# Kernel optimization log

Hardware: AMD Instinct MI355X
Metric: run time of the kernel (lower is better)

## Reference

```python
import jax, jax.numpy as jnp
from jax import lax
import numpy as np

B, N, DIM = 2, 2048, 1024
HEADS, DIM_HEAD = 16, 64
KERNELS = (0, 3, 5, 7)
GROUPS = len(KERNELS)
HPG = HEADS // GROUPS          # heads per group = 4
CG = HPG * DIM_HEAD            # channels per group for depthwise conv = 256
INNER = HEADS * DIM_HEAD       # 1024


def _alibi_slopes(n):
    # power-of-2 branch of LearnedAlibiPosBias._get_slopes (n=4 here)
    start = 2.0 ** (-(2.0 ** -(np.log2(n) - 3)))
    return np.array([start * start ** i for i in range(n)], dtype=np.float32)


def setup_inputs() -> dict:
    key = jax.random.key(0)
    ks = jax.random.split(key, 24)
    d = {}
    d['x'] = jax.random.normal(ks[0], (B, N, DIM), jnp.float32)
    d['ln_gamma'] = jnp.ones((DIM,), jnp.float32)
    d['ln_beta'] = jnp.zeros((DIM,), jnp.float32)
    d['w_qkv'] = jax.random.normal(ks[1], (3 * INNER, DIM), jnp.float32) * 0.02
    i = 2
    for p in ('q', 'k', 'v'):
        for ksz in (3, 5, 7):
            d[f'dw{p}_w{ksz}'] = jax.random.normal(ks[i], (CG, 1, ksz), jnp.float32) * 0.1; i += 1
            d[f'dw{p}_b{ksz}'] = jax.random.normal(ks[i], (CG,), jnp.float32) * 0.02; i += 1
    # learned alibi slopes, initialized to the standard ALiBi values per group
    sl = _alibi_slopes(HPG).reshape(1, HPG, 1, 1)
    d['slopes'] = jnp.asarray(np.tile(sl, (GROUPS, 1, 1, 1)))
    d['w_out'] = jax.random.normal(ks[20], (DIM, INNER), jnp.float32) * 0.02
    return d


def _dw_causal_conv(xg, w, b, ksz):
    # xg: (B, CG, N); depthwise causal conv, left pad ksz-1
    xg = jnp.pad(xg, ((0, 0), (0, 0), (ksz - 1, 0)))
    out = lax.conv_general_dilated(xg, w, (1,), 'VALID',
                                   feature_group_count=CG,
                                   dimension_numbers=('NCH', 'OIH', 'NCH'))
    return out + b[None, :, None]


def _grouped_conv(t, w3, b3, w5, b5, w7, b7):
    # t: (B, INNER, N) channels laid out head-major; group g = channels [g*CG,(g+1)*CG)
    parts = [t[:, :CG]]  # group 0: kernel_size 0 -> Identity
    for i, (w, b, ksz) in enumerate(((w3, b3, 3), (w5, b5, 5), (w7, b7, 7))):
        parts.append(_dw_causal_conv(t[:, (i + 1) * CG:(i + 2) * CG], w, b, ksz))
    out = jnp.concatenate(parts, axis=1)                      # (B, INNER, N)
    out = out.reshape(B, HEADS, DIM_HEAD, N)
    return jnp.transpose(out, (0, 1, 3, 2))                   # (B, H, N, Dh)


def _forward(x, ln_gamma, ln_beta, w_qkv,
             dwq_w3, dwq_b3, dwq_w5, dwq_b5, dwq_w7, dwq_b7,
             dwk_w3, dwk_b3, dwk_w5, dwk_b5, dwk_w7, dwk_b7,
             dwv_w3, dwv_b3, dwv_w5, dwv_b5, dwv_w7, dwv_b7,
             slopes, w_out):
    scale = DIM_HEAD ** -0.5
    mu = jnp.mean(x, axis=-1, keepdims=True)
    var = jnp.var(x, axis=-1, keepdims=True)
    h = (x - mu) * lax.rsqrt(var + 1e-5) * ln_gamma + ln_beta   # (B, N, DIM)
    qkv = jnp.einsum('bnd,ed->ben', h, w_qkv)                   # (B, 3*INNER, N)
    q, k, v = jnp.split(qkv, 3, axis=1)
    q = _grouped_conv(q, dwq_w3, dwq_b3, dwq_w5, dwq_b5, dwq_w7, dwq_b7)
    k = _grouped_conv(k, dwk_w3, dwk_b3, dwk_w5, dwk_b5, dwk_w7, dwk_b7)
    v = _grouped_conv(v, dwv_w3, dwv_b3, dwv_w5, dwv_b5, dwv_w7, dwv_b7)
    sim = jnp.einsum('bhid,bhjd->bhij', q * scale, k)           # (B, H, N, N)
    idx = jnp.arange(N)
    dist = -jnp.abs(idx[None, :] - idx[:, None]).astype(sim.dtype)  # (N, N)
    bias = slopes.reshape(HEADS, 1, 1) * dist[None]             # (H, N, N)
    sim = sim + bias[None]
    causal = idx[None, :] > idx[:, None]                        # strictly future
    sim = jnp.where(causal[None, None], -jnp.finfo(sim.dtype).max, sim)
    attn = jax.nn.softmax(sim, axis=-1)
    out = jnp.einsum('bhij,bhjd->bhid', attn, v)                # (B, H, N, Dh)
    out = jnp.transpose(out, (0, 2, 1, 3)).reshape(B, N, INNER)
    return jnp.einsum('bne,de->bnd', out, w_out)


def reference(x, ln_gamma, ln_beta, w_qkv,
              dwq_w3, dwq_b3, dwq_w5, dwq_b5, dwq_w7, dwq_b7,
              dwk_w3, dwk_b3, dwk_w5, dwk_b5, dwk_w7, dwk_b7,
              dwv_w3, dwv_b3, dwv_w5, dwv_b5, dwv_w7, dwv_b7,
              slopes, w_out):
    return _forward(x, ln_gamma, ln_beta, w_qkv,
                    dwq_w3, dwq_b3, dwq_w5, dwq_b5, dwq_w7, dwq_b7,
                    dwk_w3, dwk_b3, dwk_w5, dwk_b5, dwk_w7, dwk_b7,
                    dwv_w3, dwv_b3, dwv_w5, dwv_b5, dwv_w7, dwv_b7,
                    slopes, w_out)
```

## Files before the change

kernel.cpp:

```cpp
#include <hip/hip_runtime.h>
#include <hip/hip_bf16.h>
#include <stdint.h>

typedef __bf16 bf8 __attribute__((ext_vector_type(8)));
typedef float  f4  __attribute__((ext_vector_type(4)));

constexpr int BATCH  = 2;
constexpr int SEQ    = 2048;
constexpr int DMODEL = 1024;
constexpr int NH     = 16;
constexpr int DHEAD  = 64;
constexpr int E3     = 3072;

static __device__ __forceinline__ f4 mfma16(bf8 a, bf8 b, f4 c){
  return __builtin_amdgcn_mfma_f32_16x16x32_bf16(a, b, c, 0, 0, 0);
}
static __device__ __forceinline__ uint32_t pack2(float a, float b){
  union { __bf16 h[2]; uint32_t u; } p;
  p.h[0] = (__bf16)a; p.h[1] = (__bf16)b;
  return p.u;
}
typedef const __attribute__((address_space(1))) uint32_t g_u32;
typedef __attribute__((address_space(3))) uint32_t l_u32;
static __device__ __forceinline__ void glds16(const __bf16* g, __bf16* l){
  __builtin_amdgcn_global_load_lds((g_u32*)g, (l_u32*)l, 16, 0, 0);
}

__global__ __launch_bounds__(256) void prep_kernel(const float* __restrict__ x,
                                                   const float* __restrict__ gam,
                                                   const float* __restrict__ bet,
                                                   __bf16* __restrict__ h,
                                                   const float* __restrict__ wq,
                                                   __bf16* __restrict__ wqb){
  int bid = blockIdx.x;
  int tid = threadIdx.x;
  if(bid >= BATCH*SEQ){
    int i = ((bid - BATCH*SEQ) * 256 + tid) * 4;
    float4 v = *(const float4*)(wq + i);
    __bf16 o[4] = {(__bf16)v.x, (__bf16)v.y, (__bf16)v.z, (__bf16)v.w};
    *(uint2*)(wqb + i) = *(const uint2*)o;
    return;
  }
  int row = bid;
  const float* xr = x + (size_t)row * DMODEL;
  float4 v = *(const float4*)(xr + tid*4);
  float s = v.x + v.y + v.z + v.w;
  float ss = v.x*v.x + v.y*v.y + v.z*v.z + v.w*v.w;
#pragma unroll
  for(int m=1;m<64;m<<=1){ s += __shfl_xor(s, m); ss += __shfl_xor(ss, m); }
  __shared__ float sm[8];
  int wid = tid >> 6;
  if((tid & 63) == 0){ sm[wid] = s; sm[4+wid] = ss; }
  __syncthreads();
  s  = sm[0]+sm[1]+sm[2]+sm[3];
  ss = sm[4]+sm[5]+sm[6]+sm[7];
  float mu  = s * (1.f/DMODEL);
  float var = ss * (1.f/DMODEL) - mu*mu;
  float r = rsqrtf(var + 1e-5f);
  float4 g = *(const float4*)(gam + tid*4);
  float4 bb = *(const float4*)(bet + tid*4);
  __bf16 o[4] = { (__bf16)((v.x-mu)*r*g.x + bb.x), (__bf16)((v.y-mu)*r*g.y + bb.y),
                  (__bf16)((v.z-mu)*r*g.z + bb.z), (__bf16)((v.w-mu)*r*g.w + bb.w) };
  *(uint2*)(h + (size_t)row*DMODEL + tid*4) = *(uint2*)o;
}

template<typename CT>
__global__ __launch_bounds__(256) void gemm_nt(const __bf16* __restrict__ A,
                                               const __bf16* __restrict__ Bm,
                                               CT* __restrict__ C,
                                               int M, int Ncols, int K){
  __shared__ __align__(16) __bf16 smem[4*128*32];
  __bf16* As0 = smem;
  __bf16* Bs0 = smem + 2*128*32;
  int m0 = blockIdx.y * 128, n0 = blockIdx.x * 128;
  int tid = threadIdx.x;
  int lane = tid & 63, wid = tid >> 6;
  int quad = lane >> 4, l15 = lane & 15;
  int wm = (wid >> 1) * 64, wn = (wid & 1) * 64;
  f4 acc[4][4] = {};
  int r0 = wid*32 + (lane >> 2);
  int cofs = (lane & 3) * 8;
  const __bf16* ag = A  + (size_t)(m0 + r0) * K + cofs;
  const __bf16* bg = Bm + (size_t)(n0 + r0) * K + cofs;
  const int d0 = (wid*32)*32, d1 = (wid*32+16)*32;
  const size_t rowskip = (size_t)16 * K;
  glds16(ag,           As0 + d0);
  glds16(ag + rowskip, As0 + d1);
  glds16(bg,           Bs0 + d0);
  glds16(bg + rowskip, Bs0 + d1);
  __syncthreads();
  int cur = 0;
  for(int k0 = 0; k0 < K; k0 += 32){
    int k1 = k0 + 32;
    if(k1 < K){
      int nb = cur ^ 1;
      glds16(ag + k1,           As0 + nb*128*32 + d0);
      glds16(ag + rowskip + k1, As0 + nb*128*32 + d1);
      glds16(bg + k1,           Bs0 + nb*128*32 + d0);
      glds16(bg + rowskip + k1, Bs0 + nb*128*32 + d1);
    }
    const __bf16* AsC = As0 + cur*128*32;
    const __bf16* BsC = Bs0 + cur*128*32;
    bf8 af[4], bfr[4];
#pragma unroll
    for(int i=0;i<4;i++){
      af[i]  = *(const bf8*)&AsC[(wm + i*16 + l15)*32 + quad*8];
      bfr[i] = *(const bf8*)&BsC[(wn + i*16 + l15)*32 + quad*8];
    }
#pragma unroll
    for(int mi=0;mi<4;mi++)
#pragma unroll
      for(int ni=0;ni<4;ni++)
        acc[mi][ni] = mfma16(af[mi], bfr[ni], acc[mi][ni]);
    __syncthreads();
    cur ^= 1;
  }
  if constexpr (sizeof(CT) == 2){
    __bf16* scr = smem;
    uint32_t* sp = (uint32_t*)smem;
#pragma unroll
    for(int qq=0; qq<4; qq++){
      __syncthreads();
      if((wid>>1) == (qq>>1)){
        int mi0 = (qq & 1) * 2;
#pragma unroll
        for(int mm=0; mm<2; mm++){
          int mi = mi0 + mm;
#pragma unroll
          for(int ni=0; ni<4; ni++)
#pragma unroll
            for(int r=0; r<4; r++){
              int lr = (mi - mi0)*16 + quad*4 + r;
              scr[lr*136 + wn + ni*16 + l15] = (__bf16)acc[mi][ni][r];
            }
        }
      }
      __syncthreads();
#pragma unroll
      for(int it=0; it<2; it++){
        int idx = it*256 + tid;
        int row = idx >> 4;
        int ck  = idx & 15;
        uint4 v = { sp[row*68 + ck*4 + 0], sp[row*68 + ck*4 + 1],
                    sp[row*68 + ck*4 + 2], sp[row*68 + ck*4 + 3] };
        *(uint4*)(C + (size_t)(m0 + qq*32 + row)*Ncols + n0 + ck*8) = v;
      }
    }
  } else {
    float* scr = (float*)smem;
#pragma unroll
    for(int qq=0; qq<4; qq++){
      __syncthreads();
      if((wid>>1) == (qq>>1)){
        int mi0 = (qq & 1) * 2;
#pragma unroll
        for(int mm=0; mm<2; mm++){
          int mi = mi0 + mm;
#pragma unroll
          for(int ni=0; ni<4; ni++)
#pragma unroll
            for(int r=0; r<4; r++){
              int lr = (mi - mi0)*16 + quad*4 + r;
              scr[lr*136 + wn + ni*16 + l15] = acc[mi][ni][r];
            }
        }
      }
      __syncthreads();
#pragma unroll
      for(int it=0; it<4; it++){
        int idx = it*256 + tid;
        int row = idx >> 5;
        int ck  = idx & 31;
        float4 v = { scr[row*136 + ck*4 + 0], scr[row*136 + ck*4 + 1],
                     scr[row*136 + ck*4 + 2], scr[row*136 + ck*4 + 3] };
        *(float4*)(C + (size_t)(m0 + qq*32 + row)*Ncols + n0 + ck*4) = v;
      }
    }
  }
}

__global__ __launch_bounds__(256) void conv_kernel(const __bf16* __restrict__ qkv,
    __bf16* __restrict__ qo, __bf16* __restrict__ ko, __bf16* __restrict__ vt,
    const float* qw3,const float* qb3,const float* qw5,const float* qb5,const float* qw7,const float* qb7,
    const float* kw3,const float* kb3,const float* kw5,const float* kb5,const float* kw7,const float* kb7,
    const float* vw3,const float* vb3,const float* vw5,const float* vb5,const float* vw7,const float* vb7){
  __shared__ __align__(16) __bf16 tile[72*256];
  int nc = blockIdx.x;
  int ec = blockIdx.y;
  int b  = blockIdx.z;
  int tid = threadIdx.x;
  int n0 = nc * 64;
  {
    int rrow = tid >> 5;
    int ccol = (tid & 31) * 8;
    const __bf16* src = qkv + (size_t)b*SEQ*E3 + ec*256 + ccol;
#pragma unroll
    for(int p=0;p<9;p++){
      int row = p*8 + rrow;
      int n = n0 - 8 + row;
      uint4 v = {0u,0u,0u,0u};
      if(n >= 0) v = *(const uint4*)(src + (size_t)n*E3);
      *(uint4*)&tile[row*256 + ccol] = v;
    }
  }
  __syncthreads();
  int p = ec >> 2;
  int g = ec & 3;
  float w0=0.f,w1=0.f,w2=0.f,w3=0.f,w4=0.f,w5=0.f,w6=0.f,bias=0.f;
  if(g == 1){
    const float* wp = (p==0)? qw3 : (p==1)? kw3 : vw3;
    const float* bp = (p==0)? qb3 : (p==1)? kb3 : vb3;
    w0 = wp[tid*3+0]; w1 = wp[tid*3+1]; w2 = wp[tid*3+2]; bias = bp[tid];
  } else if(g == 2){
    const float* wp = (p==0)? qw5 : (p==1)? kw5 : vw5;
    const float* bp = (p==0)? qb5 : (p==1)? kb5 : vb5;
    w0 = wp[tid*5+0]; w1 = wp[tid*5+1]; w2 = wp[tid*5+2];
    w3 = wp[tid*5+3]; w4 = wp[tid*5+4]; bias = bp[tid];
  } else if(g == 3){
    const float* wp = (p==0)? qw7 : (p==1)? kw7 : vw7;
    const float* bp = (p==0)? qb7 : (p==1)? kb7 : vb7;
    w0 = wp[tid*7+0]; w1 = wp[tid*7+1]; w2 = wp[tid*7+2]; w3 = wp[tid*7+3];
    w4 = wp[tid*7+4]; w5 = wp[tid*7+5]; w6 = wp[tid*7+6]; bias = bp[tid];
  }
  float x0 = (float)tile[2*256 + tid];
  float x1 = (float)tile[3*256 + tid];
  float x2 = (float)tile[4*256 + tid];
  float x3 = (float)tile[5*256 + tid];
  float x4 = (float)tile[6*256 + tid];
  float x5 = (float)tile[7*256 + tid];
#define CONV_STEP(cur, o)                                                      \
  { if(g == 0)      o = (cur);                                                 \
    else if(g == 1) o = w0*x4 + w1*x5 + w2*(cur) + bias;                       \
    else if(g == 2) o = w0*x2 + w1*x3 + w2*x4 + w3*x5 + w4*(cur) + bias;       \
    else            o = w0*x0 + w1*x1 + w2*x2 + w3*x3 + w4*x4 + w5*x5          \
                        + w6*(cur) + bias;                                     \
    x0=x1; x1=x2; x2=x3; x3=x4; x4=x5; x5=(cur); }
  if(p == 2){
    uint32_t vout[32];
#pragma unroll
    for(int blk=0; blk<8; blk++){
#pragma unroll
      for(int up=0; up<4; up++){
        float ca = (float)tile[(8 + blk*8 + up*2    )*256 + tid];
        float oa; CONV_STEP(ca, oa);
        float cb = (float)tile[(8 + blk*8 + up*2 + 1)*256 + tid];
        float ob; CONV_STEP(cb, ob);
        vout[blk*4 + up] = pack2(oa, ob);
      }
    }
    __syncthreads();
    uint32_t* ot = (uint32_t*)tile;
#pragma unroll
    for(int j=0;j<32;j++) ot[tid*33 + j] = vout[j];
    __syncthreads();
#pragma unroll
    for(int it=0; it<8; it++){
      int idx = it*256 + tid;
      int ch  = idx >> 3;
      int ncq = idx & 7;
      uint4 val = { ot[ch*33 + ncq*4 + 0], ot[ch*33 + ncq*4 + 1],
                    ot[ch*33 + ncq*4 + 2], ot[ch*33 + ncq*4 + 3] };
      int hh2 = g*4 + (ch >> 6);
      int dh2 = ch & 63;
      *(uint4*)(vt + ((size_t)((b*NH + hh2)*DHEAD + dh2))*SEQ + n0 + ncq*8) = val;
    }
  } else {
    int hh = g*4 + (tid >> 6);
    int dh = tid & 63;
    __bf16* outp = (p==0) ? qo : ko;
    __bf16* op = outp + ((size_t)(b*NH + hh)*SEQ)*DHEAD + dh;
#pragma unroll 8
    for(int dn=0; dn<64; dn++){
      float cur = (float)tile[(8+dn)*256 + tid];
      float o; CONV_STEP(cur, o);
      op[(size_t)(n0+dn)*DHEAD] = (__bf16)o;
    }
  }
#undef CONV_STEP
}

__global__ __launch_bounds__(256, 3) void attn_kernel(const __bf16* __restrict__ Qin,
                                                      const __bf16* __restrict__ Kin,
                                                      const __bf16* __restrict__ Vtin,
                                                      const float* __restrict__ slopes,
                                                      __bf16* __restrict__ Oout,
                                                      const float* __restrict__ wsrc,
                                                      __bf16* __restrict__ wdst){
  __shared__ __align__(16) __bf16 Ks[2][64*64];
  __shared__ __align__(16) __bf16 Vts[2][64*64];
  __shared__ __align__(16) __bf16 Ps[4][16*72];
  __shared__ float Al[4][16];
  int bid = blockIdx.x;
  int tid = threadIdx.x;
  if(bid >= 1024){
    int i = ((bid - 1024) * 256 + tid) * 4;
    float4 v = *(const float4*)(wsrc + i);
    __bf16 o[4] = {(__bf16)v.x, (__bf16)v.y, (__bf16)v.z, (__bf16)v.w};
    *(uint2*)(wdst + i) = *(const uint2*)o;
    return;
  }
  int qi = 31 - (bid >> 5);
  int by = (bid & 7) + ((bid >> 3) & 3) * 8;
  int b  = by >> 4, hh = by & 15;
  int lane = tid & 63, w = tid >> 6;
  int quad = lane >> 4, l15 = lane & 15;
  const __bf16* qb  = Qin  + (size_t)by * SEQ * DHEAD;
  const __bf16* kb  = Kin  + (size_t)by * SEQ * DHEAD;
  const __bf16* vtb = Vtin + (size_t)by * DHEAD * SEQ;
  const float L2E = 1.4426950408889634f;
  float slope = slopes[hh];
  const float c1 = 0.125f * L2E;
  float c2 = slope * L2E;
  float cjb[16];
#pragma unroll
  for(int jt=0;jt<4;jt++)
#pragma unroll
    for(int r=0;r<4;r++)
      cjb[jt*4+r] = c2 * (float)(jt*16 + quad*4 + r);

  int sxq0 = ((quad     ^ (l15 & 7)) << 3);
  int sxq1 = (((quad+4) ^ (l15 & 7)) << 3);

  int r8 = lane >> 3;
  int c8 = lane & 7;
  int sw = (c8 ^ r8) * 8;
  const __bf16* ksrc = kb  + (size_t)r8*DHEAD + sw;
  const __bf16* vsrc = vtb + (size_t)r8*SEQ  + sw;
  int g0 = w*2, g1 = w*2 + 1;
  const size_t kg0o = (size_t)g0*8*DHEAD, kg1o = (size_t)g1*8*DHEAD;
  const size_t vg0o = (size_t)g0*8*SEQ,   vg1o = (size_t)g1*8*SEQ;

  int q0 = qi * 64;
  int nst = qi + 1;
  int i0 = q0 + w*16;
  int i  = i0 + l15;
  bf8 aq0 = *(const bf8*)(qb + (size_t)i*DHEAD + quad*8);
  bf8 aq1 = *(const bf8*)(qb + (size_t)i*DHEAD + 32 + quad*8);
  f4 oacc[4] = {};
  float l_ = 0.f;
  glds16(ksrc + kg0o, &Ks[0][g0*512]);
  glds16(ksrc + kg1o, &Ks[0][g1*512]);
  glds16(vsrc + vg0o, &Vts[0][g0*512]);
  glds16(vsrc + vg1o, &Vts[0][g1*512]);
  __syncthreads();
  int cur = 0;
  for(int t=0; t<nst; t++){
    int j0 = t*64;
    bool pf = (t+1) < nst;
    if(pf){
      int nb = cur ^ 1;
      size_t off = (size_t)(t+1)*64;
      glds16(ksrc + off*DHEAD + kg0o, &Ks[nb][g0*512]);
      glds16(ksrc + off*DHEAD + kg1o, &Ks[nb][g1*512]);
      glds16(vsrc + vg0o + off,       &Vts[nb][g0*512]);
      glds16(vsrc + vg1o + off,       &Vts[nb][g1*512]);
    }
    const __bf16* KsC  = Ks[cur];
    const __bf16* VtsC = Vts[cur];
    f4 s[4] = {};
    __builtin_amdgcn_s_setprio(1);
#pragma unroll
    for(int jt=0;jt<4;jt++){
      bf8 ak0 = *(const bf8*)&KsC[(jt*16+l15)*64 + sxq0];
      bf8 ak1 = *(const bf8*)&KsC[(jt*16+l15)*64 + sxq1];
      s[jt] = mfma16(ak0, aq0, s[jt]);
      s[jt] = mfma16(ak1, aq1, s[jt]);
    }
    __builtin_amdgcn_s_setprio(0);
    bf8 bv[2][4];
#pragma unroll
    for(int jk=0;jk<2;jk++)
#pragma unroll
      for(int nd=0;nd<4;nd++)
        bv[jk][nd] = *(const bf8*)&VtsC[(nd*16+l15)*64 + (((jk*4+quad) ^ (l15&7)) << 3)];
    float sv[4][4];
    if(t < nst-1){
      float cdi = c2 * (float)(i - j0) + 8.0f;
#pragma unroll
      for(int jt=0;jt<4;jt++)
#pragma unroll
        for(int r=0;r<4;r++)
          sv[jt][r] = fmaf(s[jt][r], c1, cjb[jt*4+r] - cdi);
    } else {
#pragma unroll
      for(int jt=0;jt<4;jt++)
#pragma unroll
        for(int r=0;r<4;r++){
          int j = j0 + jt*16 + quad*4 + r;
          int d = i - j;
          float val = fmaf(s[jt][r], c1, -fmaf(c2, (float)d, 8.0f));
          sv[jt][r] = (d < 0) ? -1e30f : val;
        }
    }
    float lsum = 0.f;
#pragma unroll
    for(int jt=0;jt<4;jt++){
      float p0 = __builtin_amdgcn_exp2f(sv[jt][0]);
      float p1 = __builtin_amdgcn_exp2f(sv[jt][1]);
      float p2 = __builtin_amdgcn_exp2f(sv[jt][2]);
      float p3 = __builtin_amdgcn_exp2f(sv[jt][3]);
      lsum += (p0+p1)+(p2+p3);
      uint2 pk = { pack2(p0,p1), pack2(p2,p3) };
      *(uint2*)&Ps[w][l15*72 + jt*16 + quad*4] = pk;
    }
    lsum += __shfl_xor(lsum, 16);
    lsum += __shfl_xor(lsum, 32);
    l_ += lsum;
    __builtin_amdgcn_s_setprio(1);
#pragma unroll
    for(int jk=0;jk<2;jk++){
      bf8 ap = *(const bf8*)&Ps[w][l15*72 + jk*32 + quad*8];
#pragma unroll
      for(int nd=0;nd<4;nd++)
        oacc[nd] = mfma16(ap, bv[jk][nd], oacc[nd]);
    }
    __builtin_amdgcn_s_setprio(0);
    __syncthreads();
    cur ^= 1;
  }
  if(quad == 0) Al[w][l15] = 1.0f / l_;
  f4 linv = *(const f4*)&Al[w][quad*4];
#pragma unroll
  for(int nd=0;nd<4;nd++)
#pragma unroll
    for(int r=0;r<4;r++){
      int io = i0 + quad*4 + r;
      Oout[((size_t)(b*SEQ + io))*DMODEL + hh*64 + nd*16 + l15] =
          (__bf16)(oacc[nd][r] * linv[r]);
    }
}

extern "C" void kernel_launch(void* const* d_in, const int* in_sizes, int n_in,
                              void* d_out, int out_size, void* d_ws, size_t ws_size,
                              hipStream_t stream){
  const float* x      = (const float*)d_in[0];
  const float* gam    = (const float*)d_in[1];
  const float* bet    = (const float*)d_in[2];
  const float* w_qkv  = (const float*)d_in[3];
  const float* slopes = (const float*)d_in[22];
  const float* w_out  = (const float*)d_in[23];
  float* out = (float*)d_out;

  char* ws = (char*)d_ws;
  __bf16* h       = (__bf16*)(ws);
  __bf16* qpost   = (__bf16*)(ws);
  __bf16* qkv     = (__bf16*)(ws + ((size_t)8  << 20));
  __bf16* att     = (__bf16*)(ws + ((size_t)8  << 20));
  __bf16* wout_bf = (__bf16*)(ws + ((size_t)24 << 20));
  __bf16* wqkv_bf = (__bf16*)(ws + ((size_t)32 << 20));
  __bf16* kpost   = (__bf16*)(ws + ((size_t)32 << 20));
  __bf16* vtp     = (__bf16*)(ws + ((size_t)40 << 20));

  constexpr int NQKV = 3 * DMODEL * DMODEL;

  prep_kernel<<<BATCH*SEQ + NQKV/4/256, 256, 0, stream>>>(x, gam, bet, h, w_qkv, wqkv_bf);
  gemm_nt<__bf16><<<dim3(E3/128, (BATCH*SEQ)/128), 256, 0, stream>>>(
      h, wqkv_bf, qkv, BATCH*SEQ, E3, DMODEL);
  conv_kernel<<<dim3(32, 12, BATCH), 256, 0, stream>>>(qkv, qpost, kpost, vtp,
    (const float*)d_in[4],(const float*)d_in[5],(const float*)d_in[6],(const float*)d_in[7],
    (const float*)d_in[8],(const float*)d_in[9],
    (const float*)d_in[10],(const float*)d_in[11],(const float*)d_in[12],(const float*)d_in[13],
    (const float*)d_in[14],(const float*)d_in[15],
    (const float*)d_in[16],(const float*)d_in[17],(const float*)d_in[18],(const float*)d_in[19],
    (const float*)d_in[20],(const float*)d_in[21]);
  attn_kernel<<<dim3(2048), 256, 0, stream>>>(qpost, kpost, vtp, slopes, att,
                                              w_out, wout_bf);
  gemm_nt<float><<<dim3(DMODEL/128, (BATCH*SEQ)/128), 256, 0, stream>>>(
      att, wout_bf, out, BATCH*SEQ, DMODEL, DMODEL);
}
```

Baseline: 234.0 us.

## Process 128-query tiles per attention block, reusing K/V tiles across two row groups

Each attention block now handles 128 query rows instead of 64, and each wave computes two 16-row query groups against the same K and V shared-memory tiles. This halves the number of attention blocks and the K/V global loads per query. It also changes the block-to-tile mapping so that heavy and light causal tiles are interleaved. The cost is more registers per wave (two accumulator sets and two score sets), which may lower occupancy, and fewer blocks in total to fill the GPU.

```diff
diff --git a/kernel.cpp b/kernel.cpp
--- a/kernel.cpp
+++ b/kernel.cpp
@@ -288,18 +288,18 @@
                                                       __bf16* __restrict__ wdst){
   __shared__ __align__(16) __bf16 Ks[2][64*64];
   __shared__ __align__(16) __bf16 Vts[2][64*64];
-  __shared__ __align__(16) __bf16 Ps[4][16*72];
-  __shared__ float Al[4][16];
+  __shared__ __align__(16) __bf16 Ps[4][2][16*72];
+  __shared__ float Al[4][2][16];
   int bid = blockIdx.x;
   int tid = threadIdx.x;
-  if(bid >= 1024){
-    int i = ((bid - 1024) * 256 + tid) * 4;
+  if(bid >= 512){
+    int i = ((bid - 512) * 256 + tid) * 4;
     float4 v = *(const float4*)(wsrc + i);
     __bf16 o[4] = {(__bf16)v.x, (__bf16)v.y, (__bf16)v.z, (__bf16)v.w};
     *(uint2*)(wdst + i) = *(const uint2*)o;
     return;
   }
-  int qi = 31 - (bid >> 5);
+  int qi = (bid < 256) ? (15 - (bid >> 5)) : ((bid >> 5) - 8);
   int by = (bid & 7) + ((bid >> 3) & 3) * 8;
   int b  = by >> 4, hh = by & 15;
   int lane = tid & 63, w = tid >> 6;
@@ -330,14 +330,16 @@
   const size_t kg0o = (size_t)g0*8*DHEAD, kg1o = (size_t)g1*8*DHEAD;
   const size_t vg0o = (size_t)g0*8*SEQ,   vg1o = (size_t)g1*8*SEQ;
 
-  int q0 = qi * 64;
-  int nst = qi + 1;
-  int i0 = q0 + w*16;
-  int i  = i0 + l15;
-  bf8 aq0 = *(const bf8*)(qb + (size_t)i*DHEAD + quad*8);
-  bf8 aq1 = *(const bf8*)(qb + (size_t)i*DHEAD + 32 + quad*8);
-  f4 oacc[4] = {};
-  float l_ = 0.f;
+  int q0 = qi * 128;
+  int nst = 2*qi + 2;
+  int ig0 = q0 + w*32 + l15;
+  int ig1 = ig0 + 16;
+  bf8 aq00 = *(const bf8*)(qb + (size_t)ig0*DHEAD + quad*8);
+  bf8 aq01 = *(const bf8*)(qb + (size_t)ig0*DHEAD + 32 + quad*8);
+  bf8 aq10 = *(const bf8*)(qb + (size_t)ig1*DHEAD + quad*8);
+  bf8 aq11 = *(const bf8*)(qb + (size_t)ig1*DHEAD + 32 + quad*8);
+  f4 oacc0[4] = {}, oacc1[4] = {};
+  float l_0 = 0.f, l_1 = 0.f;
   glds16(ksrc + kg0o, &Ks[0][g0*512]);
   glds16(ksrc + kg1o, &Ks[0][g1*512]);
   glds16(vsrc + vg0o, &Vts[0][g0*512]);
@@ -357,14 +359,16 @@
     }
     const __bf16* KsC  = Ks[cur];
     const __bf16* VtsC = Vts[cur];
-    f4 s[4] = {};
+    f4 s0[4] = {}, s1[4] = {};
     __builtin_amdgcn_s_setprio(1);
 #pragma unroll
     for(int jt=0;jt<4;jt++){
       bf8 ak0 = *(const bf8*)&KsC[(jt*16+l15)*64 + sxq0];
       bf8 ak1 = *(const bf8*)&KsC[(jt*16+l15)*64 + sxq1];
-      s[jt] = mfma16(ak0, aq0, s[jt]);
-      s[jt] = mfma16(ak1, aq1, s[jt]);
+      s0[jt] = mfma16(ak0, aq00, s0[jt]);
+      s0[jt] = mfma16(ak1, aq01, s0[jt]);
+      s1[jt] = mfma16(ak0, aq10, s1[jt]);
+      s1[jt] = mfma16(ak1, aq11, s1[jt]);
     }
     __builtin_amdgcn_s_setprio(0);
     bf8 bv[2][4];
@@ -373,60 +377,72 @@
 #pragma unroll
       for(int nd=0;nd<4;nd++)
         bv[jk][nd] = *(const bf8*)&VtsC[(nd*16+l15)*64 + (((jk*4+quad) ^ (l15&7)) << 3)];
-    float sv[4][4];
-    if(t < nst-1){
-      float cdi = c2 * (float)(i - j0) + 8.0f;
-#pragma unroll
-      for(int jt=0;jt<4;jt++)
-#pragma unroll
-        for(int r=0;r<4;r++)
-          sv[jt][r] = fmaf(s[jt][r], c1, cjb[jt*4+r] - cdi);
-    } else {
-#pragma unroll
-      for(int jt=0;jt<4;jt++)
-#pragma unroll
-        for(int r=0;r<4;r++){
-          int j = j0 + jt*16 + quad*4 + r;
-          int d = i - j;
-          float val = fmaf(s[jt][r], c1, -fmaf(c2, (float)d, 8.0f));
-          sv[jt][r] = (d < 0) ? -1e30f : val;
-        }
-    }
-    float lsum = 0.f;
-#pragma unroll
-    for(int jt=0;jt<4;jt++){
-      float p0 = __builtin_amdgcn_exp2f(sv[jt][0]);
-      float p1 = __builtin_amdgcn_exp2f(sv[jt][1]);
-      float p2 = __builtin_amdgcn_exp2f(sv[jt][2]);
-      float p3 = __builtin_amdgcn_exp2f(sv[jt][3]);
-      lsum += (p0+p1)+(p2+p3);
-      uint2 pk = { pack2(p0,p1), pack2(p2,p3) };
-      *(uint2*)&Ps[w][l15*72 + jt*16 + quad*4] = pk;
-    }
-    lsum += __shfl_xor(lsum, 16);
-    lsum += __shfl_xor(lsum, 32);
-    l_ += lsum;
+    bool masked = (t >= nst-2);
+#pragma unroll
+    for(int qg=0; qg<2; qg++){
+      const f4* sq = qg ? s1 : s0;
+      int iq = qg ? ig1 : ig0;
+      float sv[4][4];
+      if(!masked){
+        float cdi = c2 * (float)(iq - j0) + 8.0f;
+#pragma unroll
+        for(int jt=0;jt<4;jt++)
+#pragma unroll
+          for(int r=0;r<4;r++)
+            sv[jt][r] = fmaf(sq[jt][r], c1, cjb[jt*4+r] - cdi);
+      } else {
+#pragma unroll
+        for(int jt=0;jt<4;jt++)
+#pragma unroll
+          for(int r=0;r<4;r++){
+            int j = j0 + jt*16 + quad*4 + r;
+            int d = iq - j;
+            float val = fmaf(sq[jt][r], c1, -fmaf(c2, (float)d, 8.0f));
+            sv[jt][r] = (d < 0) ? -1e30f : val;
+          }
+      }
+      float lsum = 0.f;
+#pragma unroll
+      for(int jt=0;jt<4;jt++){
+        float p0 = __builtin_amdgcn_exp2f(sv[jt][0]);
+        float p1 = __builtin_amdgcn_exp2f(sv[jt][1]);
+        float p2 = __builtin_amdgcn_exp2f(sv[jt][2]);
+        float p3 = __builtin_amdgcn_exp2f(sv[jt][3]);
+        lsum += (p0+p1)+(p2+p3);
+        uint2 pk = { pack2(p0,p1), pack2(p2,p3) };
+        *(uint2*)&Ps[w][qg][l15*72 + jt*16 + quad*4] = pk;
+      }
+      lsum += __shfl_xor(lsum, 16);
+      lsum += __shfl_xor(lsum, 32);
+      if(qg) l_1 += lsum; else l_0 += lsum;
+    }
     __builtin_amdgcn_s_setprio(1);
 #pragma unroll
     for(int jk=0;jk<2;jk++){
-      bf8 ap = *(const bf8*)&Ps[w][l15*72 + jk*32 + quad*8];
-#pragma unroll
-      for(int nd=0;nd<4;nd++)
-        oacc[nd] = mfma16(ap, bv[jk][nd], oacc[nd]);
+      bf8 ap0 = *(const bf8*)&Ps[w][0][l15*72 + jk*32 + quad*8];
+      bf8 ap1 = *(const bf8*)&Ps[w][1][l15*72 + jk*32 + quad*8];
+#pragma unroll
+      for(int nd=0;nd<4;nd++){
+        oacc0[nd] = mfma16(ap0, bv[jk][nd], oacc0[nd]);
+        oacc1[nd] = mfma16(ap1, bv[jk][nd], oacc1[nd]);
+      }
     }
     __builtin_amdgcn_s_setprio(0);
     __syncthreads();
     cur ^= 1;
   }
-  if(quad == 0) Al[w][l15] = 1.0f / l_;
-  f4 linv = *(const f4*)&Al[w][quad*4];
+  if(quad == 0){ Al[w][0][l15] = 1.0f / l_0; Al[w][1][l15] = 1.0f / l_1; }
+  f4 linv0 = *(const f4*)&Al[w][0][quad*4];
+  f4 linv1 = *(const f4*)&Al[w][1][quad*4];
 #pragma unroll
   for(int nd=0;nd<4;nd++)
 #pragma unroll
     for(int r=0;r<4;r++){
-      int io = i0 + quad*4 + r;
-      Oout[((size_t)(b*SEQ + io))*DMODEL + hh*64 + nd*16 + l15] =
-          (__bf16)(oacc[nd][r] * linv[r]);
+      int io0 = q0 + w*32 + quad*4 + r;
+      Oout[((size_t)(b*SEQ + io0))*DMODEL + hh*64 + nd*16 + l15] =
+          (__bf16)(oacc0[nd][r] * linv0[r]);
+      Oout[((size_t)(b*SEQ + io0 + 16))*DMODEL + hh*64 + nd*16 + l15] =
+          (__bf16)(oacc1[nd][r] * linv1[r]);
     }
 }
 
@@ -463,7 +479,7 @@
     (const float*)d_in[14],(const float*)d_in[15],
     (const float*)d_in[16],(const float*)d_in[17],(const float*)d_in[18],(const float*)d_in[19],
     (const float*)d_in[20],(const float*)d_in[21]);
-  attn_kernel<<<dim3(2048), 256, 0, stream>>>(qpost, kpost, vtp, slopes, att,
+  attn_kernel<<<dim3(1536), 256, 0, stream>>>(qpost, kpost, vtp, slopes, att,
                                               w_out, wout_bf);
   gemm_nt<float><<<dim3(DMODEL/128, (BATCH*SEQ)/128), 256, 0, stream>>>(
       att, wout_bf, out, BATCH*SEQ, DMODEL, DMODEL);
```

Result: slower. 341.7 us (+46.0%).
